# Performance work log

Hardware: AMD Instinct MI355X
Metric: run time of the kernel (lower is better)

Reference implementation:

```python
import jax, jax.numpy as jnp
import numpy as np

NEG_SLOPE = 0.2


def gat_conv(x, src, dst, W, a_src, a_dst, bias, heads, out_ch):
    # x: [N, F_in]; src/dst: [E] (message flows src -> dst, softmax over dst)
    N = x.shape[0]
    h = (x @ W).reshape(N, heads, out_ch)              # [N, H, C]
    alpha_s = (h * a_src).sum(-1)                      # [N, H]
    alpha_d = (h * a_dst).sum(-1)                      # [N, H]
    e = jax.nn.leaky_relu(alpha_s[src] + alpha_d[dst], NEG_SLOPE)  # [E, H]
    # segment softmax over destination nodes (every node has a self loop)
    emax = jax.ops.segment_max(e, dst, num_segments=N)             # [N, H]
    ee = jnp.exp(e - emax[dst])
    denom = jax.ops.segment_sum(ee, dst, num_segments=N)           # [N, H]
    alpha = ee / denom[dst]                                        # [E, H]
    msg = h[src] * alpha[..., None]                                # [E, H, C]
    out = jax.ops.segment_sum(msg, dst, num_segments=N)            # [N, H, C]
    return out.reshape(N, heads * out_ch) + bias


def setup_inputs() -> dict:
    key = jax.random.key(0)
    ks = jax.random.split(key, 12)
    N, E, EL = 100000, 1600000, 100000
    F_in, C, H = 128, 64, 2
    glorot = lambda k, shp: jax.random.normal(k, shp, jnp.float32) * np.sqrt(2.0 / (shp[0] + shp[-1]))
    return {
        "x": jax.random.normal(ks[0], (N, F_in), jnp.float32),
        "edge_index": jax.random.randint(ks[1], (2, E), 0, N, jnp.int32),
        "edge_label_index": jax.random.randint(ks[2], (2, EL), 0, N, jnp.int32),
        "W1": glorot(ks[3], (F_in, H * C)),
        "a_src1": glorot(ks[4], (H, C)),
        "a_dst1": glorot(ks[5], (H, C)),
        "b1": jnp.zeros((H * C,), jnp.float32),
        "W2": glorot(ks[6], (H * C, C)),
        "a_src2": glorot(ks[7], (1, C)),
        "a_dst2": glorot(ks[8], (1, C)),
        "b2": jnp.zeros((C,), jnp.float32),
    }


def reference(x, edge_index, edge_label_index, W1, a_src1, a_dst1, b1, W2, a_src2, a_dst2, b2):
    N = x.shape[0]
    # add self loops (PyG GATConv default)
    loop = jnp.arange(N, dtype=edge_index.dtype)
    src = jnp.concatenate([edge_index[0], loop])
    dst = jnp.concatenate([edge_index[1], loop])
    H, C = a_src1.shape[0], a_src1.shape[1]
    z = jax.nn.elu(gat_conv(x, src, dst, W1, a_src1, a_dst1, b1, H, C))
    z = gat_conv(z, src, dst, W2, a_src2, a_dst2, b2, 1, C)         # [N, C]
    # decode: dot product of endpoint embeddings
    return (z[edge_label_index[0]] * z[edge_label_index[1]]).sum(axis=1)
```

## Files before the change

### kernel.cpp

```cpp
#include <hip/hip_runtime.h>
#include <hip/hip_bf16.h>

#define NEG_SLOPE 0.2f
#define LRELU(v) ((v) > 0.f ? (v) : NEG_SLOPE * (v))
#define BBITS 7
#define BSZ 128

typedef unsigned short ushort_t;
typedef unsigned int uint_t;
typedef float v2f __attribute__((ext_vector_type(2)));
typedef float f32x4 __attribute__((ext_vector_type(4)));
typedef short bf16x8 __attribute__((ext_vector_type(8)));

static inline int cdiv(int a, int b) { return (a + b - 1) / b; }

__device__ __forceinline__ float wsum(float v) {
#pragma unroll
    for (int o = 32; o; o >>= 1) v += __shfl_xor(v, o);
    return v;
}
__device__ __forceinline__ ushort_t f2bfbits(float f) {
    __hip_bfloat16 b = __float2bfloat16(f);
    return *reinterpret_cast<ushort_t*>(&b);
}

__global__ __launch_bounds__(256) void k_zero_int(int* p, int n) {
    int i = blockIdx.x * 256 + threadIdx.x;
    if (i < n) p[i] = 0;
}

__global__ __launch_bounds__(256) void k_bhist(const int* __restrict__ ei, int E, int ET, int NB,
                                               int* __restrict__ bcnt) {
    extern __shared__ int hist[];
    for (int i = threadIdx.x; i < NB; i += 256) hist[i] = 0;
    __syncthreads();
    int stride = gridDim.x * 256;
    for (int i = blockIdx.x * 256 + threadIdx.x; i < ET; i += stride) {
        int d = (i < E) ? ei[E + i] : (i - E);
        atomicAdd(&hist[d >> BBITS], 1);
    }
    __syncthreads();
    for (int i = threadIdx.x; i < NB; i += 256) {
        int c = hist[i];
        if (c) atomicAdd(&bcnt[i], c);
    }
}

__global__ void k_scan_small(const int* __restrict__ bcnt, int NB,
                             int* __restrict__ boff, int* __restrict__ bcur,
                             int* __restrict__ offs, int N, int ET) {
    extern __shared__ int sm[];
    for (int i = threadIdx.x; i < NB; i += blockDim.x) sm[i] = bcnt[i];
    __syncthreads();
    if (threadIdx.x == 0) {
        int run = 0;
        for (int i = 0; i < NB; i++) { int c = sm[i]; sm[i] = run; run += c; }
    }
    __syncthreads();
    for (int i = threadIdx.x; i < NB; i += blockDim.x) { boff[i] = sm[i]; bcur[i] = sm[i]; }
    if (threadIdx.x == 0) { boff[NB] = ET; offs[N] = ET; }
}

__global__ __launch_bounds__(256) void k_bscatter(const int* __restrict__ ei, int E, int ET, int NB,
                                                  int* __restrict__ bcur,
                                                  long long* __restrict__ tmp) {
    extern __shared__ int sm2[];
    int* hist = sm2;
    int* cur = sm2 + NB;
    const int CH = 4096;
    int c0 = blockIdx.x * CH;
    int c1 = min(ET, c0 + CH);
    for (int i = threadIdx.x; i < NB; i += 256) hist[i] = 0;
    __syncthreads();
    for (int i = c0 + threadIdx.x; i < c1; i += 256) {
        int d = (i < E) ? ei[E + i] : (i - E);
        atomicAdd(&hist[d >> BBITS], 1);
    }
    __syncthreads();
    for (int i = threadIdx.x; i < NB; i += 256) {
        int c = hist[i];
        cur[i] = c ? atomicAdd(&bcur[i], c) : 0;
    }
    __syncthreads();
    for (int i = c0 + threadIdx.x; i < c1; i += 256) {
        int s = (i < E) ? ei[i] : (i - E);
        int d = (i < E) ? ei[E + i] : (i - E);
        int pos = atomicAdd(&cur[d >> BBITS], 1);
        tmp[pos] = ((long long)d << 32) | (unsigned)s;
    }
}

__global__ __launch_bounds__(256) void k_csrfin(const long long* __restrict__ tmp,
                                                const int* __restrict__ boff, int NB, int N,
                                                int* __restrict__ offs, int* __restrict__ ssrc) {
    __shared__ int deg[BSZ], cur[BSZ], sc[BSZ];
    int b = blockIdx.x;
    int node0 = b << BBITS;
    int nn = min(BSZ, N - node0);
    int r0 = boff[b], r1 = boff[b + 1];
    int t = threadIdx.x;
    if (t < BSZ) deg[t] = 0;
    __syncthreads();
    for (int i = r0 + t; i < r1; i += 256) {
        int d = (int)(tmp[i] >> 32);
        atomicAdd(&deg[d - node0], 1);
    }
    __syncthreads();
    if (t < BSZ) sc[t] = deg[t];
    __syncthreads();
    for (int o = 1; o < BSZ; o <<= 1) {
        int v = 0;
        if (t < BSZ && t >= o) v = sc[t - o];
        __syncthreads();
        if (t < BSZ) sc[t] += v;
        __syncthreads();
    }
    if (t < BSZ) {
        int ex = sc[t] - deg[t];
        cur[t] = r0 + ex;
        if (t < nn) offs[node0 + t] = r0 + ex;
    }
    __syncthreads();
    for (int i = r0 + t; i < r1; i += 256) {
        long long v = tmp[i];
        int d = (int)(v >> 32);
        int s = (int)(v & 0xffffffffLL);
        int pos = atomicAdd(&cur[d - node0], 1);
        ssrc[pos] = s;
    }
}

__global__ __launch_bounds__(256) void k_wt(const float* __restrict__ W, ushort_t* __restrict__ Wt,
                                            int K, int M) {
    for (int idx = blockIdx.x * 256 + threadIdx.x; idx < K * M; idx += gridDim.x * 256) {
        int k = idx / M, n = idx % M;
        Wt[n * K + k] = f2bfbits(W[idx]);
    }
}

template <int M, int H>
__global__ __launch_bounds__(256) void k_gemm_mfma(const float* __restrict__ x,
                                                   const ushort_t* __restrict__ Wt,
                                                   const float* __restrict__ a_src,
                                                   const float* __restrict__ a_dst,
                                                   ushort_t* __restrict__ h,
                                                   float* __restrict__ as, float* __restrict__ ad,
                                                   int N) {
    constexpr int T = M / 16;
    int t = threadIdx.x;
    int w = t >> 6;
    int lane = t & 63;
    int ln = lane & 15;
    int q = lane >> 4;
    int rowA = blockIdx.x * 64 + w * 16 + ln;
    int rowD0 = blockIdx.x * 64 + w * 16 + q * 4;

    f32x4 acc[T];
#pragma unroll
    for (int i = 0; i < T; i++) acc[i] = (f32x4){0.f, 0.f, 0.f, 0.f};

#pragma unroll
    for (int kc = 0; kc < 4; kc++) {
        bf16x8 afrag;
        float xv[8];
        if (rowA < N) {
            float4 v0 = *(const float4*)(x + (size_t)rowA * 128 + kc * 32 + q * 8);
            float4 v1 = *(const float4*)(x + (size_t)rowA * 128 + kc * 32 + q * 8 + 4);
            xv[0] = v0.x; xv[1] = v0.y; xv[2] = v0.z; xv[3] = v0.w;
            xv[4] = v1.x; xv[5] = v1.y; xv[6] = v1.z; xv[7] = v1.w;
        } else {
#pragma unroll
            for (int j = 0; j < 8; j++) xv[j] = 0.f;
        }
#pragma unroll
        for (int j = 0; j < 8; j++) afrag[j] = (short)f2bfbits(xv[j]);
#pragma unroll
        for (int tt = 0; tt < T; tt++) {
            bf16x8 bfrag = *(const bf16x8*)(Wt + (size_t)(tt * 16 + ln) * 128 + kc * 32 + q * 8);
            acc[tt] = __builtin_amdgcn_mfma_f32_16x16x32_bf16(afrag, bfrag, acc[tt], 0, 0, 0);
        }
    }

#pragma unroll
    for (int tt = 0; tt < T; tt++)
#pragma unroll
        for (int r = 0; r < 4; r++) {
            int row = rowD0 + r;
            if (row < N) h[(size_t)row * M + tt * 16 + ln] = f2bfbits(acc[tt][r]);
        }

    float avs[T], avd[T];
#pragma unroll
    for (int tt = 0; tt < T; tt++) {
        avs[tt] = a_src[tt * 16 + ln];
        avd[tt] = a_dst[tt * 16 + ln];
    }
#pragma unroll
    for (int r = 0; r < 4; r++) {
        int row = rowD0 + r;
        if (H == 2) {
            float ps0 = 0.f, ps1 = 0.f, pd0 = 0.f, pd1 = 0.f;
#pragma unroll
            for (int tt = 0; tt < T / 2; tt++) { ps0 += acc[tt][r] * avs[tt]; pd0 += acc[tt][r] * avd[tt]; }
#pragma unroll
            for (int tt = T / 2; tt < T; tt++) { ps1 += acc[tt][r] * avs[tt]; pd1 += acc[tt][r] * avd[tt]; }
#pragma unroll
            for (int o = 8; o; o >>= 1) {
                ps0 += __shfl_down(ps0, o, 16); pd0 += __shfl_down(pd0, o, 16);
                ps1 += __shfl_down(ps1, o, 16); pd1 += __shfl_down(pd1, o, 16);
            }
            if (ln == 0 && row < N) {
                as[(size_t)row * 2] = ps0; as[(size_t)row * 2 + 1] = ps1;
                ad[(size_t)row * 2] = pd0; ad[(size_t)row * 2 + 1] = pd1;
            }
        } else {
            float ps = 0.f, pd = 0.f;
#pragma unroll
            for (int tt = 0; tt < T; tt++) { ps += acc[tt][r] * avs[tt]; pd += acc[tt][r] * avd[tt]; }
#pragma unroll
            for (int o = 8; o; o >>= 1) {
                ps += __shfl_down(ps, o, 16); pd += __shfl_down(pd, o, 16);
            }
            if (ln == 0 && row < N) { as[row] = ps; ad[row] = pd; }
        }
    }
}

template <int H, bool ELU_ACT>
__global__ __launch_bounds__(256) void k_agg_fused(const int* __restrict__ offs,
                                                   const int* __restrict__ ssrc,
                                                   const ushort_t* __restrict__ h,
                                                   const float* __restrict__ as,
                                                   const float* __restrict__ ad,
                                                   const float* __restrict__ bias,
                                                   float* __restrict__ z, int N) {
    constexpr int G = 16 * H;
    constexpr int EPW = 64 / G;
    constexpr int RB = H * 128;
    __shared__ uint2 meta[4][64 * H];
    int wv = threadIdx.x >> 6;
    int lane = threadIdx.x & 63;
    int d = (blockIdx.x * 256 + threadIdx.x) >> 6;
    if (d >= N) return;
    uint2* mw = meta[wv];
    int cpos = lane % G;
    int sub = lane / G;
    int hself = (H == 2) ? (cpos >> 4) : 0;
    const char* hb = (const char*)h;
    int cpo8 = cpos * 8;
    const char* mbase = (const char*)mw + ((H == 2) ? (sub * 16 + hself * 8) : (sub * 8));

    float adh[H], den[H];
#pragma unroll
    for (int hh = 0; hh < H; hh++) { adh[hh] = ad[(size_t)d * H + hh]; den[hh] = 0.f; }
    v2f acc2[2];
    acc2[0] = (v2f){0.f, 0.f};
    acc2[1] = (v2f){0.f, 0.f};

    int e0 = offs[d], e1 = offs[d + 1];
    for (int cb = e0; cb < e1; cb += 64) {
        int ne = min(64, e1 - cb);
        unsigned so = 0;
        float p[H];
#pragma unroll
        for (int hh = 0; hh < H; hh++) p[hh] = 0.f;
        if (lane < ne) {
            int s_l = ssrc[cb + lane];
            so = (unsigned)s_l * RB;
            if (H == 2) {
                float2 av = ((const float2*)as)[s_l];
                p[0] = __expf(LRELU(av.x + adh[0]));
                p[1] = __expf(LRELU(av.y + adh[1]));
            } else {
                p[0] = __expf(LRELU(as[s_l] + adh[0]));
            }
        }
#pragma unroll
        for (int hh = 0; hh < H; hh++) den[hh] += wsum(p[hh]);
        if (H == 2) {
            ((uint4*)mw)[lane] =
                make_uint4(so, __float_as_uint(p[0]), so, __float_as_uint(p[1]));
        } else {
            mw[lane] = make_uint2(so, __float_as_uint(p[0]));
        }
        int ng = (ne + EPW - 1) / EPW;
        for (int g0 = 0; g0 < ng; g0 += 4) {
            uint2 m[4];
#pragma unroll
            for (int g = 0; g < 4; g++) m[g] = *(const uint2*)(mbase + (g0 + g) * 32);
            uint2 hv[4];
#pragma unroll
            for (int g = 0; g < 4; g++) hv[g] = *(const uint2*)(hb + (m[g].x + cpo8));
#pragma unroll
            for (int g = 0; g < 4; g++) {
                float pvs = __uint_as_float(m[g].y);
                v2f pv = {pvs, pvs};
                v2f t0 = {__uint_as_float(hv[g].x << 16), __uint_as_float(hv[g].x & 0xffff0000u)};
                v2f t1 = {__uint_as_float(hv[g].y << 16), __uint_as_float(hv[g].y & 0xffff0000u)};
                acc2[0] += pv * t0;
                acc2[1] += pv * t1;
            }
        }
    }
#pragma unroll
    for (int o = G; o < 64; o <<= 1) {
        acc2[0][0] += __shfl_xor(acc2[0][0], o);
        acc2[0][1] += __shfl_xor(acc2[0][1], o);
        acc2[1][0] += __shfl_xor(acc2[1][0], o);
        acc2[1][1] += __shfl_xor(acc2[1][1], o);
    }
    if (lane < G) {
        float inv = 1.f / ((H == 2 && hself) ? den[1] : den[0]);
        float vout[4];
        vout[0] = acc2[0][0] * inv + bias[cpos * 4 + 0];
        vout[1] = acc2[0][1] * inv + bias[cpos * 4 + 1];
        vout[2] = acc2[1][0] * inv + bias[cpos * 4 + 2];
        vout[3] = acc2[1][1] * inv + bias[cpos * 4 + 3];
        if (ELU_ACT) {
#pragma unroll
            for (int i = 0; i < 4; i++) vout[i] = vout[i] > 0.f ? vout[i] : expm1f(vout[i]);
        }
        *(float4*)(z + (size_t)d * (H * 64) + cpos * 4) =
            make_float4(vout[0], vout[1], vout[2], vout[3]);
    }
}

__global__ __launch_bounds__(256) void k_decode(const int* __restrict__ eli,
                                                const float* __restrict__ z,
                                                float* __restrict__ out, int EL) {
    int wid = (blockIdx.x * 256 + threadIdx.x) >> 6;
    int lane = threadIdx.x & 63;
    int pi = wid * 2 + (lane >> 5);
    if (pi >= EL) return;
    int hl = lane & 31;
    int a = eli[pi], b = eli[EL + pi];
    float2 za = ((const float2*)(z + (size_t)a * 64))[hl];
    float2 zb = ((const float2*)(z + (size_t)b * 64))[hl];
    float p = za.x * zb.x + za.y * zb.y;
#pragma unroll
    for (int o = 16; o; o >>= 1) p += __shfl_down(p, o, 32);
    if (hl == 0) out[pi] = p;
}

extern "C" void kernel_launch(void* const* d_in, const int* in_sizes, int n_in,
                              void* d_out, int out_size, void* d_ws, size_t ws_size,
                              hipStream_t stream) {
    const float* x   = (const float*)d_in[0];
    const int*   ei  = (const int*)d_in[1];
    const int*   eli = (const int*)d_in[2];
    const float* W1  = (const float*)d_in[3];
    const float* as1 = (const float*)d_in[4];
    const float* ad1 = (const float*)d_in[5];
    const float* b1  = (const float*)d_in[6];
    const float* W2  = (const float*)d_in[7];
    const float* as2 = (const float*)d_in[8];
    const float* ad2 = (const float*)d_in[9];
    const float* b2  = (const float*)d_in[10];

    int N  = in_sizes[0] / 128;
    int E  = in_sizes[1] / 2;
    int EL = in_sizes[2] / 2;
    int ET = E + N;
    int NB = cdiv(N, BSZ);

    char* ws = (char*)d_ws;
    size_t off = 0;
    auto alloc = [&](size_t nbytes) -> void* {
        void* p = ws + off;
        off += (nbytes + 255) & ~(size_t)255;
        return p;
    };
    ushort_t* Hbuf = (ushort_t*)alloc((size_t)N * 128 * 2);
    float*    Zbuf = (float*)alloc((size_t)N * 128 * 4);
    float*    AS   = (float*)alloc((size_t)N * 2 * 4);
    float*    AD   = (float*)alloc((size_t)N * 2 * 4);
    int*      OFF  = (int*)alloc((size_t)(N + 1) * 4);
    int*      SSRC = (int*)alloc((size_t)ET * 4);
    int*      BCNT = (int*)alloc((size_t)NB * 4);
    int*      BOFF = (int*)alloc((size_t)(NB + 1) * 4);
    int*      BCUR = (int*)alloc((size_t)NB * 4);
    ushort_t* WT1  = (ushort_t*)alloc(128 * 128 * 2);
    ushort_t* WT2  = (ushort_t*)alloc(64 * 128 * 2);
    long long* TMP = (long long*)Zbuf;

    k_zero_int<<<cdiv(NB, 256), 256, 0, stream>>>(BCNT, NB);
    k_bhist<<<256, 256, NB * 4, stream>>>(ei, E, ET, NB, BCNT);
    k_scan_small<<<1, 256, NB * 4, stream>>>(BCNT, NB, BOFF, BCUR, OFF, N, ET);
    k_bscatter<<<cdiv(ET, 4096), 256, 2 * NB * 4, stream>>>(ei, E, ET, NB, BCUR, TMP);
    k_csrfin<<<NB, 256, 0, stream>>>(TMP, BOFF, NB, N, OFF, SSRC);

    k_wt<<<32, 256, 0, stream>>>(W1, WT1, 128, 128);
    k_wt<<<16, 256, 0, stream>>>(W2, WT2, 128, 64);

    k_gemm_mfma<128, 2><<<cdiv(N, 64), 256, 0, stream>>>(x, WT1, as1, ad1, Hbuf, AS, AD, N);
    k_agg_fused<2, true><<<cdiv(N, 4), 256, 0, stream>>>(OFF, SSRC, Hbuf, AS, AD, b1, Zbuf, N);

    k_gemm_mfma<64, 1><<<cdiv(N, 64), 256, 0, stream>>>(Zbuf, WT2, as2, ad2, Hbuf, AS, AD, N);
    k_agg_fused<1, false><<<cdiv(N, 4), 256, 0, stream>>>(OFF, SSRC, Hbuf, AS, AD, b2, Zbuf, N);

    k_decode<<<cdiv(EL, 8), 256, 0, stream>>>(eli, Zbuf, (float*)d_out, EL);
}
```

Before: 365.1 us.

## Pack CSR temp keys to 32 bits, split edge-weight precompute, store layer-1 output as bf16

Result: slower. 388.4 us (+6.4%).

```diff
diff --git a/kernel.cpp b/kernel.cpp
--- a/kernel.cpp
+++ b/kernel.cpp
@@ -63,11 +63,11 @@
 
 __global__ __launch_bounds__(256) void k_bscatter(const int* __restrict__ ei, int E, int ET, int NB,
                                                   int* __restrict__ bcur,
-                                                  long long* __restrict__ tmp) {
+                                                  uint_t* __restrict__ tmp) {
     extern __shared__ int sm2[];
     int* hist = sm2;
     int* cur = sm2 + NB;
-    const int CH = 4096;
+    const int CH = 8192;
     int c0 = blockIdx.x * CH;
     int c1 = min(ET, c0 + CH);
     for (int i = threadIdx.x; i < NB; i += 256) hist[i] = 0;
@@ -86,11 +86,11 @@
         int s = (i < E) ? ei[i] : (i - E);
         int d = (i < E) ? ei[E + i] : (i - E);
         int pos = atomicAdd(&cur[d >> BBITS], 1);
-        tmp[pos] = ((long long)d << 32) | (unsigned)s;
-    }
-}
-
-__global__ __launch_bounds__(256) void k_csrfin(const long long* __restrict__ tmp,
+        tmp[pos] = ((uint_t)(d & (BSZ - 1)) << 25) | (uint_t)s;
+    }
+}
+
+__global__ __launch_bounds__(256) void k_csrfin(const uint_t* __restrict__ tmp,
                                                 const int* __restrict__ boff, int NB, int N,
                                                 int* __restrict__ offs, int* __restrict__ ssrc) {
     __shared__ int deg[BSZ], cur[BSZ], sc[BSZ];
@@ -102,8 +102,8 @@
     if (t < BSZ) deg[t] = 0;
     __syncthreads();
     for (int i = r0 + t; i < r1; i += 256) {
-        int d = (int)(tmp[i] >> 32);
-        atomicAdd(&deg[d - node0], 1);
+        int dloc = (int)(tmp[i] >> 25);
+        atomicAdd(&deg[dloc], 1);
     }
     __syncthreads();
     if (t < BSZ) sc[t] = deg[t];
@@ -122,10 +122,10 @@
     }
     __syncthreads();
     for (int i = r0 + t; i < r1; i += 256) {
-        long long v = tmp[i];
-        int d = (int)(v >> 32);
-        int s = (int)(v & 0xffffffffLL);
-        int pos = atomicAdd(&cur[d - node0], 1);
+        uint_t v = tmp[i];
+        int dloc = (int)(v >> 25);
+        int s = (int)(v & 0x1FFFFFFu);
+        int pos = atomicAdd(&cur[dloc], 1);
         ssrc[pos] = s;
     }
 }
@@ -138,8 +138,8 @@
     }
 }
 
-template <int M, int H>
-__global__ __launch_bounds__(256) void k_gemm_mfma(const float* __restrict__ x,
+template <int M, int H, bool INBF16>
+__global__ __launch_bounds__(256) void k_gemm_mfma(const void* __restrict__ xin,
                                                    const ushort_t* __restrict__ Wt,
                                                    const float* __restrict__ a_src,
                                                    const float* __restrict__ a_dst,
@@ -162,18 +162,27 @@
 #pragma unroll
     for (int kc = 0; kc < 4; kc++) {
         bf16x8 afrag;
-        float xv[8];
-        if (rowA < N) {
-            float4 v0 = *(const float4*)(x + (size_t)rowA * 128 + kc * 32 + q * 8);
-            float4 v1 = *(const float4*)(x + (size_t)rowA * 128 + kc * 32 + q * 8 + 4);
-            xv[0] = v0.x; xv[1] = v0.y; xv[2] = v0.z; xv[3] = v0.w;
-            xv[4] = v1.x; xv[5] = v1.y; xv[6] = v1.z; xv[7] = v1.w;
+        if (INBF16) {
+            if (rowA < N)
+                afrag = *(const bf16x8*)((const ushort_t*)xin + (size_t)rowA * 128 + kc * 32 + q * 8);
+            else
+#pragma unroll
+                for (int j = 0; j < 8; j++) afrag[j] = 0;
         } else {
-#pragma unroll
-            for (int j = 0; j < 8; j++) xv[j] = 0.f;
-        }
-#pragma unroll
-        for (int j = 0; j < 8; j++) afrag[j] = (short)f2bfbits(xv[j]);
+            float xv[8];
+            if (rowA < N) {
+                const float* xf = (const float*)xin;
+                float4 v0 = *(const float4*)(xf + (size_t)rowA * 128 + kc * 32 + q * 8);
+                float4 v1 = *(const float4*)(xf + (size_t)rowA * 128 + kc * 32 + q * 8 + 4);
+                xv[0] = v0.x; xv[1] = v0.y; xv[2] = v0.z; xv[3] = v0.w;
+                xv[4] = v1.x; xv[5] = v1.y; xv[6] = v1.z; xv[7] = v1.w;
+            } else {
+#pragma unroll
+                for (int j = 0; j < 8; j++) xv[j] = 0.f;
+            }
+#pragma unroll
+            for (int j = 0; j < 8; j++) afrag[j] = (short)f2bfbits(xv[j]);
+        }
 #pragma unroll
         for (int tt = 0; tt < T; tt++) {
             bf16x8 bfrag = *(const bf16x8*)(Wt + (size_t)(tt * 16 + ln) * 128 + kc * 32 + q * 8);
@@ -226,23 +235,51 @@
     }
 }
 
-template <int H, bool ELU_ACT>
+template <int H>
+__global__ __launch_bounds__(256) void k_meta(const int* __restrict__ offs,
+                                              const int* __restrict__ ssrc,
+                                              const float* __restrict__ as,
+                                              const float* __restrict__ ad,
+                                              uint2* __restrict__ meta0,
+                                              float* __restrict__ meta1, int N) {
+    constexpr int RB = H * 128;
+    int d = (blockIdx.x * 256 + threadIdx.x) >> 6;
+    int lane = threadIdx.x & 63;
+    if (d >= N) return;
+    float adh0 = ad[(size_t)d * H];
+    float adh1 = (H == 2) ? ad[(size_t)d * H + 1] : 0.f;
+    int e0 = offs[d], e1 = offs[d + 1];
+    for (int i = e0 + lane; i < e1; i += 64) {
+        int s = ssrc[i];
+        unsigned so = (unsigned)s * RB;
+        if (H == 2) {
+            float2 av = ((const float2*)as)[s];
+            float p0 = __expf(LRELU(av.x + adh0));
+            float p1 = __expf(LRELU(av.y + adh1));
+            meta0[i] = make_uint2(so, __float_as_uint(p0));
+            meta1[i] = p1;
+        } else {
+            float p0 = __expf(LRELU(as[s] + adh0));
+            meta0[i] = make_uint2(so, __float_as_uint(p0));
+        }
+    }
+}
+
+template <int H, bool ELU_ACT, bool OUT_BF16>
 __global__ __launch_bounds__(256) void k_agg_fused(const int* __restrict__ offs,
-                                                   const int* __restrict__ ssrc,
+                                                   const uint2* __restrict__ meta0,
+                                                   const float* __restrict__ meta1,
                                                    const ushort_t* __restrict__ h,
-                                                   const float* __restrict__ as,
-                                                   const float* __restrict__ ad,
                                                    const float* __restrict__ bias,
-                                                   float* __restrict__ z, int N) {
+                                                   void* __restrict__ z, int N) {
     constexpr int G = 16 * H;
     constexpr int EPW = 64 / G;
-    constexpr int RB = H * 128;
-    __shared__ uint2 meta[4][64 * H];
+    __shared__ __align__(16) uint2 lmeta[4][64 * H];
     int wv = threadIdx.x >> 6;
     int lane = threadIdx.x & 63;
     int d = (blockIdx.x * 256 + threadIdx.x) >> 6;
     if (d >= N) return;
-    uint2* mw = meta[wv];
+    uint2* mw = lmeta[wv];
     int cpos = lane % G;
     int sub = lane / G;
     int hself = (H == 2) ? (cpos >> 4) : 0;
@@ -250,9 +287,7 @@
     int cpo8 = cpos * 8;
     const char* mbase = (const char*)mw + ((H == 2) ? (sub * 16 + hself * 8) : (sub * 8));
 
-    float adh[H], den[H];
-#pragma unroll
-    for (int hh = 0; hh < H; hh++) { adh[hh] = ad[(size_t)d * H + hh]; den[hh] = 0.f; }
+    float denp[2] = {0.f, 0.f};
     v2f acc2[2];
     acc2[0] = (v2f){0.f, 0.f};
     acc2[1] = (v2f){0.f, 0.f};
@@ -260,28 +295,19 @@
     int e0 = offs[d], e1 = offs[d + 1];
     for (int cb = e0; cb < e1; cb += 64) {
         int ne = min(64, e1 - cb);
-        unsigned so = 0;
-        float p[H];
-#pragma unroll
-        for (int hh = 0; hh < H; hh++) p[hh] = 0.f;
-        if (lane < ne) {
-            int s_l = ssrc[cb + lane];
-            so = (unsigned)s_l * RB;
-            if (H == 2) {
-                float2 av = ((const float2*)as)[s_l];
-                p[0] = __expf(LRELU(av.x + adh[0]));
-                p[1] = __expf(LRELU(av.y + adh[1]));
-            } else {
-                p[0] = __expf(LRELU(as[s_l] + adh[0]));
-            }
-        }
-#pragma unroll
-        for (int hh = 0; hh < H; hh++) den[hh] += wsum(p[hh]);
+        int i = cb + lane;
         if (H == 2) {
-            ((uint4*)mw)[lane] =
-                make_uint4(so, __float_as_uint(p[0]), so, __float_as_uint(p[1]));
+            uint2 m0 = meta0[i];
+            float p1v = meta1[i];
+            if (lane >= ne) { m0.x = 0u; m0.y = 0u; p1v = 0.f; }
+            denp[0] += __uint_as_float(m0.y);
+            denp[1] += p1v;
+            ((uint4*)mw)[lane] = make_uint4(m0.x, m0.y, m0.x, __float_as_uint(p1v));
         } else {
-            mw[lane] = make_uint2(so, __float_as_uint(p[0]));
+            uint2 m0 = meta0[i];
+            if (lane >= ne) { m0.x = 0u; m0.y = 0u; }
+            denp[0] += __uint_as_float(m0.y);
+            mw[lane] = m0;
         }
         int ng = (ne + EPW - 1) / EPW;
         for (int g0 = 0; g0 < ng; g0 += 4) {
@@ -309,8 +335,10 @@
         acc2[1][0] += __shfl_xor(acc2[1][0], o);
         acc2[1][1] += __shfl_xor(acc2[1][1], o);
     }
+    float den0 = wsum(denp[0]);
+    float den1 = (H == 2) ? wsum(denp[1]) : den0;
     if (lane < G) {
-        float inv = 1.f / ((H == 2 && hself) ? den[1] : den[0]);
+        float inv = 1.f / ((H == 2 && hself) ? den1 : den0);
         float vout[4];
         vout[0] = acc2[0][0] * inv + bias[cpos * 4 + 0];
         vout[1] = acc2[0][1] * inv + bias[cpos * 4 + 1];
@@ -320,8 +348,15 @@
 #pragma unroll
             for (int i = 0; i < 4; i++) vout[i] = vout[i] > 0.f ? vout[i] : expm1f(vout[i]);
         }
-        *(float4*)(z + (size_t)d * (H * 64) + cpos * 4) =
-            make_float4(vout[0], vout[1], vout[2], vout[3]);
+        if (OUT_BF16) {
+            ushort4 pk;
+            pk.x = f2bfbits(vout[0]); pk.y = f2bfbits(vout[1]);
+            pk.z = f2bfbits(vout[2]); pk.w = f2bfbits(vout[3]);
+            *(ushort4*)((ushort_t*)z + (size_t)d * (H * 64) + cpos * 4) = pk;
+        } else {
+            *(float4*)((float*)z + (size_t)d * (H * 64) + cpos * 4) =
+                make_float4(vout[0], vout[1], vout[2], vout[3]);
+        }
     }
 }
 
@@ -371,7 +406,7 @@
         return p;
     };
     ushort_t* Hbuf = (ushort_t*)alloc((size_t)N * 128 * 2);
-    float*    Zbuf = (float*)alloc((size_t)N * 128 * 4);
+    char*     Zbuf = (char*)alloc((size_t)N * 128 * 2);
     float*    AS   = (float*)alloc((size_t)N * 2 * 4);
     float*    AD   = (float*)alloc((size_t)N * 2 * 4);
     int*      OFF  = (int*)alloc((size_t)(N + 1) * 4);
@@ -381,22 +416,26 @@
     int*      BCUR = (int*)alloc((size_t)NB * 4);
     ushort_t* WT1  = (ushort_t*)alloc(128 * 128 * 2);
     ushort_t* WT2  = (ushort_t*)alloc(64 * 128 * 2);
-    long long* TMP = (long long*)Zbuf;
+    uint2*    MT0  = (uint2*)alloc((size_t)ET * 8 + 1024);
+    float*    MT1  = (float*)alloc((size_t)ET * 4 + 1024);
+    uint_t*   TMP  = (uint_t*)Zbuf;
 
     k_zero_int<<<cdiv(NB, 256), 256, 0, stream>>>(BCNT, NB);
     k_bhist<<<256, 256, NB * 4, stream>>>(ei, E, ET, NB, BCNT);
     k_scan_small<<<1, 256, NB * 4, stream>>>(BCNT, NB, BOFF, BCUR, OFF, N, ET);
-    k_bscatter<<<cdiv(ET, 4096), 256, 2 * NB * 4, stream>>>(ei, E, ET, NB, BCUR, TMP);
+    k_bscatter<<<cdiv(ET, 8192), 256, 2 * NB * 4, stream>>>(ei, E, ET, NB, BCUR, TMP);
     k_csrfin<<<NB, 256, 0, stream>>>(TMP, BOFF, NB, N, OFF, SSRC);
 
     k_wt<<<32, 256, 0, stream>>>(W1, WT1, 128, 128);
     k_wt<<<16, 256, 0, stream>>>(W2, WT2, 128, 64);
 
-    k_gemm_mfma<128, 2><<<cdiv(N, 64), 256, 0, stream>>>(x, WT1, as1, ad1, Hbuf, AS, AD, N);
-    k_agg_fused<2, true><<<cdiv(N, 4), 256, 0, stream>>>(OFF, SSRC, Hbuf, AS, AD, b1, Zbuf, N);
-
-    k_gemm_mfma<64, 1><<<cdiv(N, 64), 256, 0, stream>>>(Zbuf, WT2, as2, ad2, Hbuf, AS, AD, N);
-    k_agg_fused<1, false><<<cdiv(N, 4), 256, 0, stream>>>(OFF, SSRC, Hbuf, AS, AD, b2, Zbuf, N);
-
-    k_decode<<<cdiv(EL, 8), 256, 0, stream>>>(eli, Zbuf, (float*)d_out, EL);
-}
+    k_gemm_mfma<128, 2, false><<<cdiv(N, 64), 256, 0, stream>>>(x, WT1, as1, ad1, Hbuf, AS, AD, N);
+    k_meta<2><<<cdiv(N, 4), 256, 0, stream>>>(OFF, SSRC, AS, AD, MT0, MT1, N);
+    k_agg_fused<2, true, true><<<cdiv(N, 4), 256, 0, stream>>>(OFF, MT0, MT1, Hbuf, b1, Zbuf, N);
+
+    k_gemm_mfma<64, 1, true><<<cdiv(N, 64), 256, 0, stream>>>(Zbuf, WT2, as2, ad2, Hbuf, AS, AD, N);
+    k_meta<1><<<cdiv(N, 4), 256, 0, stream>>>(OFF, SSRC, AS, AD, MT0, MT1, N);
+    k_agg_fused<1, false, false><<<cdiv(N, 4), 256, 0, stream>>>(OFF, MT0, MT1, Hbuf, b2, Zbuf, N);
+
+    k_decode<<<cdiv(EL, 8), 256, 0, stream>>>(eli, (const float*)Zbuf, (float*)d_out, EL);
+}
```
